# Optimization experiments

Hardware: AMD Instinct MI355X
Metric: run time of the kernel (lower is better)

The kernel has to match this reference:

```python
import jax, jax.numpy as jnp
import numpy as np

STATE_LEN = 4096
SEQ_LEN = 8192
T = 1024  # number of time buckets in time_sim_mat


def setup_inputs() -> dict:
    key = jax.random.key(0)
    k1, k2, k3 = jax.random.split(key, 3)
    his = jax.random.randint(k1, (SEQ_LEN,), 0, T, dtype=jnp.int64 if jax.config.jax_enable_x64 else jnp.int32)
    cur = jax.random.randint(k2, (STATE_LEN,), 0, T, dtype=jnp.int64 if jax.config.jax_enable_x64 else jnp.int32)
    time_sim_mat = jax.random.normal(k3, (T, T), dtype=jnp.float32)
    return {"his": his, "cur": cur, "time_sim_mat": time_sim_mat}


def reference(his, cur, time_sim_mat):
    # attn_energies[i, j] = time_sim_mat[cur[i], his[j]]  (vectorized gather)
    energies = time_sim_mat[cur[:, None], his[None, :]]  # [state_len, seq_len]
    return jax.nn.softmax(energies, axis=-1)
```

## Files before the change

### kernel.cpp

```cpp
#include <hip/hip_runtime.h>
#include <cstddef>

#define TDIM 1024
#define SEQ 8192
#define NROWS 4096

__global__ __launch_bounds__(256) void hist_kernel(const int* __restrict__ his,
                                                   int* __restrict__ counts) {
    __shared__ int lc[TDIM];
    const int tid = threadIdx.x;
    for (int t = tid; t < TDIM; t += 256) lc[t] = 0;
    __syncthreads();
    const int base = blockIdx.x * 1024;
    for (int i = tid; i < 1024; i += 256) {
        int h = his[base + i];
        atomicAdd(&lc[h], 1);
    }
    __syncthreads();
    for (int t = tid; t < TDIM; t += 256) {
        int c = lc[t];
        if (c) atomicAdd(&counts[t], c);
    }
}

__global__ __launch_bounds__(256) void softmax_gather_kernel(
    const int* __restrict__ his, const int* __restrict__ cur,
    const float* __restrict__ M, const int* __restrict__ counts,
    float* __restrict__ out)
{
    __shared__ float prob[TDIM];
    __shared__ float red[16];
    const int tid = threadIdx.x;
    const int row = blockIdx.x;
    const int r = cur[row];
    const float* Mrow = M + (size_t)r * TDIM;

    float m[4];
    int   c[4];
#pragma unroll
    for (int k = 0; k < 4; ++k) {
        int t = tid + 256 * k;
        m[k] = Mrow[t];
        c[k] = counts[t];
    }

    float lmax = -3.402823466e38f;
#pragma unroll
    for (int k = 0; k < 4; ++k)
        if (c[k] > 0) lmax = fmaxf(lmax, m[k]);
#pragma unroll
    for (int off = 32; off > 0; off >>= 1)
        lmax = fmaxf(lmax, __shfl_down(lmax, off, 64));
    const int wave = tid >> 6, lane = tid & 63;
    if (lane == 0) red[wave] = lmax;
    __syncthreads();
    if (tid == 0) {
        float g = red[0];
        for (int w = 1; w < 4; ++w) g = fmaxf(g, red[w]);
        red[8] = g;
    }
    __syncthreads();
    const float gmax = red[8];

    float e[4];
    float lsum = 0.f;
#pragma unroll
    for (int k = 0; k < 4; ++k) {
        e[k] = __expf(m[k] - gmax);
        lsum += (float)c[k] * e[k];
    }
#pragma unroll
    for (int off = 32; off > 0; off >>= 1)
        lsum += __shfl_down(lsum, off, 64);
    if (lane == 0) red[4 + wave] = lsum;
    __syncthreads();
    if (tid == 0) {
        float s = red[4] + red[5] + red[6] + red[7];
        red[9] = 1.0f / s;
    }
    __syncthreads();
    const float inv = red[9];

#pragma unroll
    for (int k = 0; k < 4; ++k)
        prob[tid + 256 * k] = e[k] * inv;
    __syncthreads();

    const int4* his4 = (const int4*)his;
    float4* out4 = (float4*)(out + (size_t)row * SEQ);
#pragma unroll
    for (int it = 0; it < 8; ++it) {
        int j4 = it * 256 + tid;
        int4 h = his4[j4];
        float4 o;
        o.x = prob[h.x];
        o.y = prob[h.y];
        o.z = prob[h.z];
        o.w = prob[h.w];
        out4[j4] = o;
    }
}

extern "C" void kernel_launch(void* const* d_in, const int* in_sizes, int n_in,
                              void* d_out, int out_size, void* d_ws, size_t ws_size,
                              hipStream_t stream) {
    const int*   his = (const int*)d_in[0];
    const int*   cur = (const int*)d_in[1];
    const float* M   = (const float*)d_in[2];
    float* out = (float*)d_out;
    int* counts = (int*)d_ws;

    hipMemsetAsync(counts, 0, TDIM * sizeof(int), stream);
    hist_kernel<<<8, 256, 0, stream>>>(his, counts);
    softmax_gather_kernel<<<NROWS, 256, 0, stream>>>(his, cur, M, counts, out);
}
```

Baseline: 148.2 us.

## Precompute per-bucket softmax table and gather two output rows per block

Softmax normalization now runs once per distinct time bucket (1024 rows) into a workspace table P, instead of once per output row (4096). The gather kernel then loads two table rows into shared memory as interleaved float2 and writes two output rows per block, reusing each his load. The histogram becomes a single 1024-thread block that writes counts directly, which removes the memset and global atomics. The cost is an extra kernel launch and a 4 MB workspace table that must be written and then read back.

```diff
diff --git a/kernel.cpp b/kernel.cpp
--- a/kernel.cpp
+++ b/kernel.cpp
@@ -5,34 +5,25 @@
 #define SEQ 8192
 #define NROWS 4096
 
-__global__ __launch_bounds__(256) void hist_kernel(const int* __restrict__ his,
-                                                   int* __restrict__ counts) {
+__global__ __launch_bounds__(1024) void hist_kernel(const int* __restrict__ his,
+                                                    int* __restrict__ counts) {
     __shared__ int lc[TDIM];
     const int tid = threadIdx.x;
-    for (int t = tid; t < TDIM; t += 256) lc[t] = 0;
+    lc[tid] = 0;
     __syncthreads();
-    const int base = blockIdx.x * 1024;
-    for (int i = tid; i < 1024; i += 256) {
-        int h = his[base + i];
-        atomicAdd(&lc[h], 1);
-    }
+#pragma unroll
+    for (int k = 0; k < 8; ++k)
+        atomicAdd(&lc[his[tid + 1024 * k]], 1);
     __syncthreads();
-    for (int t = tid; t < TDIM; t += 256) {
-        int c = lc[t];
-        if (c) atomicAdd(&counts[t], c);
-    }
+    counts[tid] = lc[tid];
 }
 
-__global__ __launch_bounds__(256) void softmax_gather_kernel(
-    const int* __restrict__ his, const int* __restrict__ cur,
-    const float* __restrict__ M, const int* __restrict__ counts,
-    float* __restrict__ out)
-{
-    __shared__ float prob[TDIM];
+__global__ __launch_bounds__(256) void table_kernel(const float* __restrict__ M,
+                                                    const int* __restrict__ counts,
+                                                    float* __restrict__ P) {
     __shared__ float red[16];
     const int tid = threadIdx.x;
-    const int row = blockIdx.x;
-    const int r = cur[row];
+    const int r = blockIdx.x;
     const float* Mrow = M + (size_t)r * TDIM;
 
     float m[4];
@@ -55,8 +46,7 @@
     if (lane == 0) red[wave] = lmax;
     __syncthreads();
     if (tid == 0) {
-        float g = red[0];
-        for (int w = 1; w < 4; ++w) g = fmaxf(g, red[w]);
+        float g = fmaxf(fmaxf(red[0], red[1]), fmaxf(red[2], red[3]));
         red[8] = g;
     }
     __syncthreads();
@@ -74,30 +64,51 @@
         lsum += __shfl_down(lsum, off, 64);
     if (lane == 0) red[4 + wave] = lsum;
     __syncthreads();
-    if (tid == 0) {
-        float s = red[4] + red[5] + red[6] + red[7];
-        red[9] = 1.0f / s;
-    }
+    if (tid == 0) red[9] = 1.0f / (red[4] + red[5] + red[6] + red[7]);
     __syncthreads();
     const float inv = red[9];
 
+    float* Prow = P + (size_t)r * TDIM;
 #pragma unroll
     for (int k = 0; k < 4; ++k)
-        prob[tid + 256 * k] = e[k] * inv;
+        Prow[tid + 256 * k] = e[k] * inv;
+}
+
+__global__ __launch_bounds__(256) void gather_kernel(const int* __restrict__ his,
+                                                     const int* __restrict__ cur,
+                                                     const float* __restrict__ P,
+                                                     float* __restrict__ out) {
+    __shared__ float2 probs2[TDIM];
+    const int tid = threadIdx.x;
+    const int row0 = blockIdx.x * 2;
+    const int r0 = cur[row0];
+    const int r1 = cur[row0 + 1];
+
+    const float4* P0 = (const float4*)(P + (size_t)r0 * TDIM);
+    const float4* P1 = (const float4*)(P + (size_t)r1 * TDIM);
+    float4 a = P0[tid];
+    float4 b = P1[tid];
+    probs2[4 * tid + 0] = make_float2(a.x, b.x);
+    probs2[4 * tid + 1] = make_float2(a.y, b.y);
+    probs2[4 * tid + 2] = make_float2(a.z, b.z);
+    probs2[4 * tid + 3] = make_float2(a.w, b.w);
     __syncthreads();
 
     const int4* his4 = (const int4*)his;
-    float4* out4 = (float4*)(out + (size_t)row * SEQ);
+    float4* out0 = (float4*)(out + (size_t)row0 * SEQ);
+    float4* out1 = (float4*)(out + (size_t)(row0 + 1) * SEQ);
 #pragma unroll
     for (int it = 0; it < 8; ++it) {
         int j4 = it * 256 + tid;
         int4 h = his4[j4];
-        float4 o;
-        o.x = prob[h.x];
-        o.y = prob[h.y];
-        o.z = prob[h.z];
-        o.w = prob[h.w];
-        out4[j4] = o;
+        float2 px = probs2[h.x];
+        float2 py = probs2[h.y];
+        float2 pz = probs2[h.z];
+        float2 pw = probs2[h.w];
+        float4 o0 = make_float4(px.x, py.x, pz.x, pw.x);
+        float4 o1 = make_float4(px.y, py.y, pz.y, pw.y);
+        out0[j4] = o0;
+        out1[j4] = o1;
     }
 }
 
@@ -108,9 +119,11 @@
     const int*   cur = (const int*)d_in[1];
     const float* M   = (const float*)d_in[2];
     float* out = (float*)d_out;
-    int* counts = (int*)d_ws;
 
-    hipMemsetAsync(counts, 0, TDIM * sizeof(int), stream);
-    hist_kernel<<<8, 256, 0, stream>>>(his, counts);
-    softmax_gather_kernel<<<NROWS, 256, 0, stream>>>(his, cur, M, counts, out);
+    float* P      = (float*)d_ws;
+    int*   counts = (int*)((char*)d_ws + (size_t)TDIM * TDIM * 4);
+
+    hist_kernel<<<1, 1024, 0, stream>>>(his, counts);
+    table_kernel<<<TDIM, 256, 0, stream>>>(M, counts, P);
+    gather_kernel<<<NROWS / 2, 256, 0, stream>>>(his, cur, P, out);
 }
```

Result: no change. 148.8 us (+0.4%).
